# Performance work log

Measured on AMD Instinct MI355X. Metric: run time of the kernel, lower is better.

The kernel has to match this reference:

```python
import jax, jax.numpy as jnp
import numpy as np

N = 50000
E = 800000
IN_DIM, HID, OUT_DIM, HEADS = 256, 128, 64, 4


def _segment_sum(vals, ids, n):
    return jax.ops.segment_sum(vals, ids, num_segments=n)


def gcn_conv(x, src, dst, W, b, n):
    # PyG GCNConv: add self loops, symmetric normalization, aggregate at dst
    xw = x @ W  # [N, HID]
    loop = jnp.arange(n, dtype=src.dtype)
    srcA = jnp.concatenate([src, loop])
    dstA = jnp.concatenate([dst, loop])
    deg = _segment_sum(jnp.ones_like(srcA, dtype=xw.dtype), dstA, n)
    dinv = jnp.where(deg > 0, jax.lax.rsqrt(deg), 0.0)
    norm = dinv[srcA] * dinv[dstA]  # [E+N]
    msg = xw[srcA] * norm[:, None]  # [E+N, HID] -- dominant memory traffic
    return _segment_sum(msg, dstA, n) + b


def layer_norm(h, gamma, beta, eps=1e-5):
    mu = jnp.mean(h, axis=-1, keepdims=True)
    var = jnp.mean(jnp.square(h - mu), axis=-1, keepdims=True)
    return (h - mu) * jax.lax.rsqrt(var + eps) * gamma + beta


def gat_conv(x, src, dst, W, att_src, att_dst, b, n):
    # PyG GATConv (concat=True), self-loops added, eval mode (no dropout)
    xw = (x @ W).reshape(n, HEADS, HID)  # [N, H, C]
    a_s = jnp.sum(xw * att_src, axis=-1)  # [N, H]
    a_d = jnp.sum(xw * att_dst, axis=-1)  # [N, H]
    loop = jnp.arange(n, dtype=src.dtype)
    srcA = jnp.concatenate([src, loop])
    dstA = jnp.concatenate([dst, loop])
    e = jax.nn.leaky_relu(a_s[srcA] + a_d[dstA], 0.2)  # [E+N, H]
    m = jax.ops.segment_max(e, dstA, num_segments=n)  # [N, H]
    ex = jnp.exp(e - m[dstA])
    denom = _segment_sum(ex, dstA, n)  # [N, H] (>=1 entry per node via self loop)
    alpha = ex / denom[dstA]  # [E+N, H]
    msg = xw[srcA] * alpha[:, :, None]  # [E+N, H, C]
    out = _segment_sum(msg, dstA, n)  # [N, H, C]
    return out.reshape(n, HEADS * HID) + b


def setup_inputs() -> dict:
    key = jax.random.key(0)
    ks = jax.random.split(key, 16)
    x = jax.random.normal(ks[0], (N, IN_DIM), dtype=jnp.float32)
    edge_index = jax.random.randint(ks[1], (2, E), 0, N, dtype=jnp.int64)
    s = lambda k, shape, fan: jax.random.normal(k, shape, jnp.float32) / np.sqrt(fan)
    return {
        "x": x,
        "edge_index": edge_index,
        "Win": s(ks[2], (IN_DIM, HID), IN_DIM),
        "bin_": jnp.zeros((HID,), jnp.float32),
        "Wg1": s(ks[3], (HID, HID), HID),
        "bg1": jnp.zeros((HID,), jnp.float32),
        "g1_gamma": jnp.ones((HID,), jnp.float32),
        "g1_beta": jnp.zeros((HID,), jnp.float32),
        "Wg2": s(ks[4], (HID, HID), HID),
        "bg2": jnp.zeros((HID,), jnp.float32),
        "g2_gamma": jnp.ones((HID,), jnp.float32),
        "g2_beta": jnp.zeros((HID,), jnp.float32),
        "Wgat": s(ks[5], (HID, HEADS * HID), HID),
        "att_src": s(ks[6], (HEADS, HID), HID),
        "att_dst": s(ks[7], (HEADS, HID), HID),
        "bgat": jnp.zeros((HEADS * HID,), jnp.float32),
        "Watt_out": s(ks[8], (HEADS * HID, HID), HEADS * HID),
        "batt_out": jnp.zeros((HID,), jnp.float32),
        "Wout": s(ks[9], (HID, OUT_DIM), HID),
        "bout": jnp.zeros((OUT_DIM,), jnp.float32),
    }


def reference(x, edge_index, Win, bin_, Wg1, bg1, g1_gamma, g1_beta,
              Wg2, bg2, g2_gamma, g2_beta, Wgat, att_src, att_dst, bgat,
              Watt_out, batt_out, Wout, bout):
    src, dst = edge_index[0], edge_index[1]
    n = x.shape[0]
    # input projection (dropout = identity in eval)
    h0 = jax.nn.relu(x @ Win + bin_)
    # NOTE: original zip truncates -> only 2 of the 3 GCN layers execute.
    # layer 0 (i==0: no residual)
    h = gcn_conv(h0, src, dst, Wg1, bg1, n)
    h = jax.nn.relu(layer_norm(h, g1_gamma, g1_beta))
    x1 = h
    # layer 1 (i==1: residual)
    h = gcn_conv(x1, src, dst, Wg2, bg2, n)
    h = jax.nn.relu(layer_norm(h, g2_gamma, g2_beta))
    x2 = x1 + h
    # GAT attention block
    a = gat_conv(x2, src, dst, Wgat, att_src, att_dst, bgat, n)
    a = jax.nn.relu(a @ Watt_out + batt_out)
    # output projection
    return a @ Wout + bout
```

## Files before the change

kernel.cpp:

```cpp
#include <hip/hip_runtime.h>
#include <hip/hip_bf16.h>
#include <cstddef>
#include <cstdint>

#define TPB 256
#define HID 128
#define GATD 512
#define HEADS 4

typedef __attribute__((ext_vector_type(8))) short bf16x8;
typedef __attribute__((ext_vector_type(4))) float f32x4;

__device__ __forceinline__ float lrelu02(float x) { return x > 0.0f ? x : 0.2f * x; }

__device__ __forceinline__ unsigned short f2bf_rn(float f) {
  uint32_t u = __float_as_uint(f);
  u += 0x7fff + ((u >> 16) & 1);
  return (unsigned short)(u >> 16);
}
__device__ __forceinline__ float bf2f(unsigned short h) {
  return __uint_as_float(((uint32_t)h) << 16);
}
__device__ __forceinline__ float bflo(uint32_t u) { return __uint_as_float(u << 16); }
__device__ __forceinline__ float bfhi(uint32_t u) { return __uint_as_float(u & 0xffff0000u); }

__global__ void k_zero(int* __restrict__ p, int n) {
  int i = blockIdx.x * blockDim.x + threadIdx.x;
  if (i < n) p[i] = 0;
}

__global__ void k_hist(const int* __restrict__ dst, int* __restrict__ cnt, int E) {
  int i = blockIdx.x * blockDim.x + threadIdx.x;
  if (i < E) atomicAdd(&cnt[dst[i]], 1);
}

__global__ __launch_bounds__(256) void k_scan_blk(const int* __restrict__ cnt,
                                                  int* __restrict__ rowp,
                                                  int* __restrict__ bsum,
                                                  float* __restrict__ dinv, int n) {
  __shared__ int wsum[4];
  const int tid = threadIdx.x, lane = tid & 63, wid = tid >> 6;
  const int base = blockIdx.x * 1024 + tid * 4;
  int v[4];
#pragma unroll
  for (int q = 0; q < 4; ++q) {
    int idx = base + q;
    v[q] = (idx < n) ? cnt[idx] : 0;
    if (idx < n) dinv[idx] = rsqrtf((float)(v[q] + 1));
  }
  int s = v[0] + v[1] + v[2] + v[3];
  int sc = s;
#pragma unroll
  for (int off = 1; off < 64; off <<= 1) {
    int t = __shfl_up(sc, off);
    if (lane >= off) sc += t;
  }
  if (lane == 63) wsum[wid] = sc;
  __syncthreads();
  int woff = 0;
#pragma unroll
  for (int w = 0; w < 4; ++w)
    if (w < wid) woff += wsum[w];
  int run = woff + sc - s;
#pragma unroll
  for (int q = 0; q < 4; ++q) {
    int idx = base + q;
    if (idx < n) rowp[idx] = run;
    run += v[q];
  }
  if (tid == 255) bsum[blockIdx.x] = woff + sc;
}

__global__ __launch_bounds__(256) void k_scan_top(int* __restrict__ bsum, int nb) {
  __shared__ int sm[256];
  const int tid = threadIdx.x;
  int v = (tid < nb) ? bsum[tid] : 0;
  sm[tid] = v;
  __syncthreads();
  for (int off = 1; off < 256; off <<= 1) {
    int t = (tid >= off) ? sm[tid - off] : 0;
    __syncthreads();
    sm[tid] += t;
    __syncthreads();
  }
  int incl = sm[tid];
  if (tid < nb) bsum[tid] = incl - v;
  if (tid == nb - 1) bsum[nb] = incl;
}

__global__ void k_scan_add(int* __restrict__ rowp, const int* __restrict__ bsum,
                           int n, int nb) {
  int i = blockIdx.x * blockDim.x + threadIdx.x;
  if (i < n) rowp[i] += bsum[i >> 10];
  if (i == 0) rowp[n] = bsum[nb];
}

__global__ void k_fill(const int* __restrict__ src, const int* __restrict__ dst,
                       const int* __restrict__ rowp, int* __restrict__ cur,
                       int* __restrict__ colsrc, int E) {
  int i = blockIdx.x * blockDim.x + threadIdx.x;
  if (i < E) {
    int d = dst[i];
    int pos = rowp[d] + atomicAdd(&cur[d], 1);
    colsrc[pos] = src[i];
  }
}

__global__ void k_splitw_all(const float* __restrict__ Win, const float* __restrict__ Wg1,
                             const float* __restrict__ Wg2, const float* __restrict__ Wout,
                             unsigned short* __restrict__ WinTh, unsigned short* __restrict__ WinTl,
                             unsigned short* __restrict__ Wg1Th, unsigned short* __restrict__ Wg1Tl,
                             unsigned short* __restrict__ Wg2Th, unsigned short* __restrict__ Wg2Tl,
                             unsigned short* __restrict__ WoutTh, unsigned short* __restrict__ WoutTl) {
  int t = blockIdx.x * blockDim.x + threadIdx.x;
  const float* W;
  unsigned short *H, *L;
  int K, NC, r;
  if (t < 32768)      { W = Win;  H = WinTh;  L = WinTl;  K = 256; NC = 128; r = t; }
  else if (t < 49152) { W = Wg1;  H = Wg1Th;  L = Wg1Tl;  K = 128; NC = 128; r = t - 32768; }
  else if (t < 65536) { W = Wg2;  H = Wg2Th;  L = Wg2Tl;  K = 128; NC = 128; r = t - 49152; }
  else if (t < 73728) { W = Wout; H = WoutTh; L = WoutTl; K = 128; NC = 64;  r = t - 65536; }
  else return;
  int k = r / NC, n2 = r % NC;
  float v = W[r];
  unsigned short h = f2bf_rn(v);
  H[(size_t)n2 * K + k] = h;
  L[(size_t)n2 * K + k] = f2bf_rn(v - bf2f(h));
}

__global__ __launch_bounds__(256) void k_vprep(const float* __restrict__ Wgat,
                                               const float* __restrict__ Wao,
                                               unsigned short* __restrict__ VTh,
                                               unsigned short* __restrict__ VTl) {
  int t = blockIdx.x * blockDim.x + threadIdx.x;
  if (t >= 512 * 128) return;
  int j = t >> 7, k = t & 127;
  int c = j >> 2, h = j & 3;
  const float* wg = Wgat + (size_t)k * GATD + h * HID;
  const float* wa = Wao + (size_t)(h * HID) * HID + c;
  float s = 0.f;
#pragma unroll 4
  for (int d = 0; d < HID; ++d) s = fmaf(wg[d], wa[(size_t)d * HID], s);
  unsigned short hi = f2bf_rn(s);
  VTh[(size_t)j * HID + k] = hi;
  VTl[(size_t)j * HID + k] = f2bf_rn(s - bf2f(hi));
}

__global__ void k_cbias(const float* __restrict__ bgat, const float* __restrict__ Wao,
                        const float* __restrict__ bao, float* __restrict__ cb) {
  int c = threadIdx.x;
  if (c >= HID) return;
  float s = bao[c];
  for (int d = 0; d < GATD; ++d) s = fmaf(bgat[d], Wao[(size_t)d * HID + c], s);
  cb[c] = s;
}

template <int KTOT, int KC, int NCB, bool RELU, bool BIAS, int OUTM, int AMODE>
__global__ __launch_bounds__(256) void k_gemm5(
    const unsigned short* __restrict__ Ah, const unsigned short* __restrict__ Al,
    const unsigned short* __restrict__ BhT, const unsigned short* __restrict__ BlT,
    const float* __restrict__ bias, void* __restrict__ Cv, void* __restrict__ Cv2,
    int M, int NC) {
  constexpr int NSUB = KC / 32;
  constexpr int NCHUNK = KTOT / KC;
  constexpr int NCF = NCB / 16;
  constexpr int UNITS = NSUB * 2 * 4 * NCB;
  __shared__ alignas(16) unsigned short Bs[NSUB][2][4][NCB][8];
  const int tid = threadIdx.x, lane = tid & 63, wid = tid >> 6;
  const int m0 = blockIdx.x * 64;
  const int n0 = blockIdx.y * NCB;
  const int fr = lane & 15, g = lane >> 4;
  const int arow = m0 + wid * 16 + fr;
  const bool aok = arow < M;
  const size_t abase = (size_t)arow * KTOT;

  f32x4 acc[NCF];
#pragma unroll
  for (int cf = 0; cf < NCF; ++cf) acc[cf] = (f32x4){0.f, 0.f, 0.f, 0.f};

  for (int c = 0; c < NCHUNK; ++c) {
    const int c0 = c * KC;
    if (c > 0) __syncthreads();
#pragma unroll
    for (int it = 0; it < UNITS / 256; ++it) {
      const int u = tid + it * 256;
      const int n = u % NCB;
      int rest = u / NCB;
      const int kg = rest & 3;
      rest >>= 2;
      const int p = rest & 1;
      const int sub = rest >> 1;
      const unsigned short* sp =
          (p ? BlT : BhT) + (size_t)(n0 + n) * KTOT + c0 + sub * 32 + kg * 8;
      *(uint4*)&Bs[sub][p][kg][n][0] = *(const uint4*)sp;
    }
    __syncthreads();
#pragma unroll
    for (int sub = 0; sub < NSUB; ++sub) {
      const int kb = c0 + sub * 32 + g * 8;
      bf16x8 a_h = {}, a_l = {};
      if (aok) {
        if (AMODE == 0) {
          a_h = *(const bf16x8*)(Ah + abase + kb);
          a_l = *(const bf16x8*)(Al + abase + kb);
        } else {
          const float* Af = (const float*)Ah + abase + kb;
          float4 q0 = *(const float4*)Af;
          float4 q1 = *(const float4*)(Af + 4);
          float av[8] = {q0.x, q0.y, q0.z, q0.w, q1.x, q1.y, q1.z, q1.w};
          union { bf16x8 v; uint32_t u4[4]; } Hu, Lu;
#pragma unroll
          for (int q = 0; q < 4; ++q) {
            unsigned short h0 = f2bf_rn(av[2 * q]);
            unsigned short h1 = f2bf_rn(av[2 * q + 1]);
            unsigned short l0 = f2bf_rn(av[2 * q] - bf2f(h0));
            unsigned short l1 = f2bf_rn(av[2 * q + 1] - bf2f(h1));
            Hu.u4[q] = (uint32_t)h0 | ((uint32_t)h1 << 16);
            Lu.u4[q] = (uint32_t)l0 | ((uint32_t)l1 << 16);
          }
          a_h = Hu.v;
          a_l = Lu.v;
        }
      }
#pragma unroll
      for (int cf = 0; cf < NCF; ++cf) {
        bf16x8 b_h = *(const bf16x8*)&Bs[sub][0][g][cf * 16 + fr][0];
        bf16x8 b_l = *(const bf16x8*)&Bs[sub][1][g][cf * 16 + fr][0];
        acc[cf] = __builtin_amdgcn_mfma_f32_16x16x32_bf16(a_h, b_h, acc[cf], 0, 0, 0);
        acc[cf] = __builtin_amdgcn_mfma_f32_16x16x32_bf16(a_h, b_l, acc[cf], 0, 0, 0);
        acc[cf] = __builtin_amdgcn_mfma_f32_16x16x32_bf16(a_l, b_h, acc[cf], 0, 0, 0);
      }
    }
  }
#pragma unroll
  for (int cf = 0; cf < NCF; ++cf) {
    const int col = n0 + cf * 16 + fr;
    const float bv = BIAS ? bias[col] : 0.f;
#pragma unroll
    for (int r = 0; r < 4; ++r) {
      const int grow = m0 + wid * 16 + g * 4 + r;
      if (grow < M) {
        float v = acc[cf][r] + bv;
        if (RELU) v = fmaxf(v, 0.f);
        const size_t idx = (size_t)grow * NC + col;
        if (OUTM == 0) {
          ((float*)Cv)[idx] = v;
        } else if (OUTM == 1) {
          ((unsigned short*)Cv)[idx] = f2bf_rn(v);
        } else {
          unsigned short h = f2bf_rn(v);
          ((unsigned short*)Cv)[idx] = h;
          ((unsigned short*)Cv2)[idx] = f2bf_rn(v - bf2f(h));
        }
      }
    }
  }
}

template <bool L2>
__global__ __launch_bounds__(256) void k_gcn_agg(
    const unsigned short* __restrict__ xwb, const float* __restrict__ dinv,
    const int* __restrict__ rowp, const int* __restrict__ colsrc,
    const float* __restrict__ bias, const float* __restrict__ gamma,
    const float* __restrict__ beta,
    const unsigned short* __restrict__ resh, const unsigned short* __restrict__ resl,
    unsigned short* __restrict__ oh, unsigned short* __restrict__ ol,
    const float* __restrict__ waT, float* __restrict__ a_s, float* __restrict__ a_d,
    int n) {
  __shared__ float w[8][HID];
  if (L2) {
    for (int t = threadIdx.x; t < 8 * HID; t += 256) ((float*)w)[t] = waT[t];
    __syncthreads();
  }
  const int lane = threadIdx.x & 63;
  const int i = blockIdx.x * 4 + (threadIdx.x >> 6);
  if (i >= n) return;
  const float di = dinv[i];
  const int c = lane * 2;
  uint32_t v0 = *(const uint32_t*)(xwb + (size_t)i * HID + c);
  float a0 = bflo(v0) * di * di, a1 = bfhi(v0) * di * di;
  float b0 = 0.f, b1 = 0.f;
  const int e0 = rowp[i], e1 = rowp[i + 1];
  int j = e0;
  for (; j + 3 < e1; j += 4) {
    int s0 = colsrc[j], s1 = colsrc[j + 1], s2 = colsrc[j + 2], s3 = colsrc[j + 3];
    float w0 = dinv[s0] * di, w1 = dinv[s1] * di, w2 = dinv[s2] * di, w3 = dinv[s3] * di;
    uint32_t u0 = *(const uint32_t*)(xwb + (size_t)s0 * HID + c);
    uint32_t u1 = *(const uint32_t*)(xwb + (size_t)s1 * HID + c);
    uint32_t u2 = *(const uint32_t*)(xwb + (size_t)s2 * HID + c);
    uint32_t u3 = *(const uint32_t*)(xwb + (size_t)s3 * HID + c);
    a0 = fmaf(bflo(u0), w0, a0); a1 = fmaf(bfhi(u0), w0, a1);
    b0 = fmaf(bflo(u1), w1, b0); b1 = fmaf(bfhi(u1), w1, b1);
    a0 = fmaf(bflo(u2), w2, a0); a1 = fmaf(bfhi(u2), w2, a1);
    b0 = fmaf(bflo(u3), w3, b0); b1 = fmaf(bfhi(u3), w3, b1);
  }
  for (; j < e1; ++j) {
    int s0 = colsrc[j];
    float w0 = dinv[s0] * di;
    uint32_t u0 = *(const uint32_t*)(xwb + (size_t)s0 * HID + c);
    a0 = fmaf(bflo(u0), w0, a0);
    a1 = fmaf(bfhi(u0), w0, a1);
  }
  a0 += b0;
  a1 += b1;
  a0 += bias[c];
  a1 += bias[c + 1];
  float s1 = a0 + a1, s2 = a0 * a0 + a1 * a1;
#pragma unroll
  for (int m = 32; m >= 1; m >>= 1) {
    s1 += __shfl_xor(s1, m);
    s2 += __shfl_xor(s2, m);
  }
  float mu = s1 * (1.0f / HID);
  float var = s2 * (1.0f / HID) - mu * mu;
  float rstd = rsqrtf(var + 1e-5f);
  float y0 = fmaxf((a0 - mu) * rstd * gamma[c] + beta[c], 0.0f);
  float y1 = fmaxf((a1 - mu) * rstd * gamma[c + 1] + beta[c + 1], 0.0f);
  if (L2) {
    uint32_t rh = *(const uint32_t*)(resh + (size_t)i * HID + c);
    uint32_t rl = *(const uint32_t*)(resl + (size_t)i * HID + c);
    y0 += bflo(rh) + bflo(rl);
    y1 += bfhi(rh) + bfhi(rl);
  }
  unsigned short ph0 = f2bf_rn(y0), ph1 = f2bf_rn(y1);
  uint32_t hw = (uint32_t)ph0 | ((uint32_t)ph1 << 16);
  uint32_t lw = (uint32_t)f2bf_rn(y0 - bf2f(ph0)) |
                ((uint32_t)f2bf_rn(y1 - bf2f(ph1)) << 16);
  *(uint32_t*)(oh + (size_t)i * HID + c) = hw;
  *(uint32_t*)(ol + (size_t)i * HID + c) = lw;
  if (L2) {
    float p[8];
#pragma unroll
    for (int h = 0; h < 8; ++h) p[h] = y0 * w[h][c] + y1 * w[h][c + 1];
#pragma unroll
    for (int m = 32; m >= 1; m >>= 1) {
#pragma unroll
      for (int h = 0; h < 8; ++h) p[h] += __shfl_xor(p[h], m);
    }
    if (lane == 0) {
      a_s[i * 4 + 0] = p[0]; a_s[i * 4 + 1] = p[1];
      a_s[i * 4 + 2] = p[2]; a_s[i * 4 + 3] = p[3];
      a_d[i * 4 + 0] = p[4]; a_d[i * 4 + 1] = p[5];
      a_d[i * 4 + 2] = p[6]; a_d[i * 4 + 3] = p[7];
    }
  }
}

__global__ __launch_bounds__(256) void k_wprep(const float* __restrict__ Wgat,
                                               const float* __restrict__ att_src,
                                               const float* __restrict__ att_dst,
                                               float* __restrict__ waT) {
  int t = blockIdx.x * blockDim.x + threadIdx.x;
  if (t >= 1024) return;
  int p = t >> 7, k = t & 127;
  int h = p & 3;
  const float* av = (p < 4 ? att_src : att_dst) + h * HID;
  const float* wrow = Wgat + (size_t)k * GATD + h * HID;
  float s = 0.f;
#pragma unroll 4
  for (int c = 0; c < HID; ++c) s = fmaf(wrow[c], av[c], s);
  waT[t] = s;
}

__global__ __launch_bounds__(256) void k_gat_agg2(const unsigned short* __restrict__ zb,
                                                  const float* __restrict__ a_s,
                                                  const float* __restrict__ a_d,
                                                  const int* __restrict__ rowp,
                                                  const int* __restrict__ colsrc,
                                                  const float* __restrict__ cb,
                                                  unsigned short* __restrict__ atth,
                                                  unsigned short* __restrict__ attl,
                                                  int n) {
  __shared__ float4 albuf[4][64];
  __shared__ int sbuf[4][64];
  const int lane = threadIdx.x & 63;
  const int wid = threadIdx.x >> 6;
  const int i = blockIdx.x * 4 + wid;
  if (i >= n) return;
  const float4 adv = *(const float4*)(a_d + i * 4);
  const float4 asv = *(const float4*)(a_s + i * 4);
  float es0 = lrelu02(asv.x + adv.x);
  float es1 = lrelu02(asv.y + adv.y);
  float es2 = lrelu02(asv.z + adv.z);
  float es3 = lrelu02(asv.w + adv.w);
  const int e0 = rowp[i], e1 = rowp[i + 1];
  float m0 = es0, m1 = es1, m2 = es2, m3 = es3;
  for (int j = e0 + lane; j < e1; j += 64) {
    int s = colsrc[j];
    const float4 av = *(const float4*)(a_s + s * 4);
    m0 = fmaxf(m0, lrelu02(av.x + adv.x));
    m1 = fmaxf(m1, lrelu02(av.y + adv.y));
    m2 = fmaxf(m2, lrelu02(av.z + adv.z));
    m3 = fmaxf(m3, lrelu02(av.w + adv.w));
  }
#pragma unroll
  for (int m = 32; m >= 1; m >>= 1) {
    m0 = fmaxf(m0, __shfl_xor(m0, m));
    m1 = fmaxf(m1, __shfl_xor(m1, m));
    m2 = fmaxf(m2, __shfl_xor(m2, m));
    m3 = fmaxf(m3, __shfl_xor(m3, m));
  }
  float d0 = 0.f, d1 = 0.f, d2 = 0.f, d3 = 0.f;
  for (int j = e0 + lane; j < e1; j += 64) {
    int s = colsrc[j];
    const float4 av = *(const float4*)(a_s + s * 4);
    d0 += __expf(lrelu02(av.x + adv.x) - m0);
    d1 += __expf(lrelu02(av.y + adv.y) - m1);
    d2 += __expf(lrelu02(av.z + adv.z) - m2);
    d3 += __expf(lrelu02(av.w + adv.w) - m3);
  }
#pragma unroll
  for (int m = 32; m >= 1; m >>= 1) {
    d0 += __shfl_xor(d0, m);
    d1 += __shfl_xor(d1, m);
    d2 += __shfl_xor(d2, m);
    d3 += __shfl_xor(d3, m);
  }
  d0 += __expf(es0 - m0);
  d1 += __expf(es1 - m1);
  d2 += __expf(es2 - m2);
  d3 += __expf(es3 - m3);
  const float inv0 = 1.0f / d0, inv1 = 1.0f / d1, inv2 = 1.0f / d2, inv3 = 1.0f / d3;
  const float4 asf = make_float4(__expf(es0 - m0) * inv0, __expf(es1 - m1) * inv1,
                                 __expf(es2 - m2) * inv2, __expf(es3 - m3) * inv3);
  const int col8 = lane * 8;
  uint4 u = *(const uint4*)(zb + (size_t)i * GATD + col8);
  float4 accC0 = make_float4(bflo(u.x) * asf.x, bfhi(u.x) * asf.y,
                             bflo(u.y) * asf.z, bfhi(u.y) * asf.w);
  float4 accC1 = make_float4(bflo(u.z) * asf.x, bfhi(u.z) * asf.y,
                             bflo(u.w) * asf.z, bfhi(u.w) * asf.w);
  for (int b = e0; b < e1; b += 64) {
    int j = b + lane;
    if (j < e1) {
      int s = colsrc[j];
      const float4 av = *(const float4*)(a_s + s * 4);
      albuf[wid][lane] = make_float4(__expf(lrelu02(av.x + adv.x) - m0) * inv0,
                                     __expf(lrelu02(av.y + adv.y) - m1) * inv1,
                                     __expf(lrelu02(av.z + adv.z) - m2) * inv2,
                                     __expf(lrelu02(av.w + adv.w) - m3) * inv3);
      sbuf[wid][lane] = s;
    }
    asm volatile("s_waitcnt lgkmcnt(0)" ::: "memory");
    const int cnt = min(64, e1 - b);
    for (int t = 0; t < cnt; ++t) {
      float4 a4 = albuf[wid][t];
      int s = sbuf[wid][t];
      uint4 w = *(const uint4*)(zb + (size_t)s * GATD + col8);
      accC0.x = fmaf(bflo(w.x), a4.x, accC0.x);
      accC0.y = fmaf(bfhi(w.x), a4.y, accC0.y);
      accC0.z = fmaf(bflo(w.y), a4.z, accC0.z);
      accC0.w = fmaf(bfhi(w.y), a4.w, accC0.w);
      accC1.x = fmaf(bflo(w.z), a4.x, accC1.x);
      accC1.y = fmaf(bfhi(w.z), a4.y, accC1.y);
      accC1.z = fmaf(bflo(w.w), a4.z, accC1.z);
      accC1.w = fmaf(bfhi(w.w), a4.w, accC1.w);
    }
  }
  const int c0 = lane * 2;
  float2 cbv = *(const float2*)(cb + c0);
  float o0 = fmaxf(accC0.x + accC0.y + accC0.z + accC0.w + cbv.x, 0.0f);
  float o1 = fmaxf(accC1.x + accC1.y + accC1.z + accC1.w + cbv.y, 0.0f);
  unsigned short ph0 = f2bf_rn(o0), ph1 = f2bf_rn(o1);
  uint32_t hw = (uint32_t)ph0 | ((uint32_t)ph1 << 16);
  uint32_t lw = (uint32_t)f2bf_rn(o0 - bf2f(ph0)) |
                ((uint32_t)f2bf_rn(o1 - bf2f(ph1)) << 16);
  *(uint32_t*)(atth + (size_t)i * HID + c0) = hw;
  *(uint32_t*)(attl + (size_t)i * HID + c0) = lw;
}

extern "C" void kernel_launch(void* const* d_in, const int* in_sizes, int n_in,
                              void* d_out, int out_size, void* d_ws, size_t ws_size,
                              hipStream_t stream) {
  const float* x = (const float*)d_in[0];
  const int* ei = (const int*)d_in[1];
  const float* Win = (const float*)d_in[2];
  const float* bin = (const float*)d_in[3];
  const float* Wg1 = (const float*)d_in[4];
  const float* bg1 = (const float*)d_in[5];
  const float* g1g = (const float*)d_in[6];
  const float* g1b = (const float*)d_in[7];
  const float* Wg2 = (const float*)d_in[8];
  const float* bg2 = (const float*)d_in[9];
  const float* g2g = (const float*)d_in[10];
  const float* g2b = (const float*)d_in[11];
  const float* Wgat = (const float*)d_in[12];
  const float* att_s = (const float*)d_in[13];
  const float* att_d = (const float*)d_in[14];
  const float* bgat = (const float*)d_in[15];
  const float* Wao = (const float*)d_in[16];
  const float* bao = (const float*)d_in[17];
  const float* Wout = (const float*)d_in[18];
  const float* bout = (const float*)d_in[19];

  const int N = in_sizes[0] / 256;
  const int E = in_sizes[1] / 2;
  const int* src = ei;
  const int* dst = ei + E;

  char* base = (char*)d_ws;
  size_t off = 0;
  unsigned short* h0h = (unsigned short*)(base + off); off += (size_t)N * HID * 2;
  unsigned short* h0l = (unsigned short*)(base + off); off += (size_t)N * HID * 2;
  unsigned short* x1h = (unsigned short*)(base + off); off += (size_t)N * HID * 2;
  unsigned short* x1l = (unsigned short*)(base + off); off += (size_t)N * HID * 2;
  unsigned short* xwb = (unsigned short*)(base + off); off += (size_t)N * HID * 2;
  unsigned short* x2h = (unsigned short*)(base + off); off += (size_t)N * HID * 2;
  unsigned short* x2l = (unsigned short*)(base + off); off += (size_t)N * HID * 2;
  unsigned short* atth = x2h;
  unsigned short* attl = x2l;
  unsigned short* zb = (unsigned short*)(base + off); off += (size_t)N * GATD * 2;
  float* dinv = (float*)(base + off);                 off += (size_t)N * 4;
  float* a_s = (float*)(base + off);                  off += (size_t)N * 16;
  float* a_d = (float*)(base + off);                  off += (size_t)N * 16;
  float* waT = (float*)(base + off);                  off += 4096;
  float* cb = (float*)(base + off);                   off += 512;
  unsigned short *WinTh, *WinTl, *Wg1Th, *Wg1Tl, *Wg2Th, *Wg2Tl, *WoutTh, *WoutTl;
  unsigned short *VTh, *VTl;
  WinTh = (unsigned short*)(base + off);  off += 256 * 128 * 2;
  WinTl = (unsigned short*)(base + off);  off += 256 * 128 * 2;
  Wg1Th = (unsigned short*)(base + off);  off += 128 * 128 * 2;
  Wg1Tl = (unsigned short*)(base + off);  off += 128 * 128 * 2;
  Wg2Th = (unsigned short*)(base + off);  off += 128 * 128 * 2;
  Wg2Tl = (unsigned short*)(base + off);  off += 128 * 128 * 2;
  VTh = (unsigned short*)(base + off);    off += 512 * 128 * 2;
  VTl = (unsigned short*)(base + off);    off += 512 * 128 * 2;
  WoutTh = (unsigned short*)(base + off); off += 128 * 64 * 2;
  WoutTl = (unsigned short*)(base + off); off += 128 * 64 * 2;
  int* rowp = (int*)(base + off);   off += (size_t)(N + 1) * 4;
  int* colsrc = (int*)(base + off); off += (size_t)E * 4;
  const int nb2 = (N + 1023) / 1024;
  int* bsum = (int*)(base + off);   off += (size_t)(nb2 + 2) * 4;
  int* cnt = (int*)zb;
  int* cur = cnt + N;

  const int eb = (E + TPB - 1) / TPB;
  const int zbk = (2 * N + TPB - 1) / TPB;
  const int ab = (N + 3) / 4;
  const int gm = (N + 63) / 64;

  k_zero<<<zbk, TPB, 0, stream>>>(cnt, 2 * N);
  k_hist<<<eb, TPB, 0, stream>>>(dst, cnt, E);
  k_scan_blk<<<nb2, 256, 0, stream>>>(cnt, rowp, bsum, dinv, N);
  k_scan_top<<<1, 256, 0, stream>>>(bsum, nb2);
  k_scan_add<<<(N + 255) / 256, 256, 0, stream>>>(rowp, bsum, N, nb2);
  k_fill<<<eb, TPB, 0, stream>>>(src, dst, rowp, cur, colsrc, E);
  k_wprep<<<4, 256, 0, stream>>>(Wgat, att_s, att_d, waT);
  k_vprep<<<256, 256, 0, stream>>>(Wgat, Wao, VTh, VTl);
  k_cbias<<<1, 128, 0, stream>>>(bgat, Wao, bao, cb);
  k_splitw_all<<<(73728 + 255) / 256, 256, 0, stream>>>(
      Win, Wg1, Wg2, Wout, WinTh, WinTl, Wg1Th, Wg1Tl, Wg2Th, Wg2Tl, WoutTh, WoutTl);

  k_gemm5<256, 64, 128, true, true, 2, 1><<<dim3(gm, 1), 256, 0, stream>>>(
      (const unsigned short*)x, nullptr, WinTh, WinTl, bin, h0h, h0l, N, 128);
  k_gemm5<128, 64, 128, false, false, 1, 0><<<dim3(gm, 1), 256, 0, stream>>>(
      h0h, h0l, Wg1Th, Wg1Tl, nullptr, xwb, nullptr, N, 128);
  k_gcn_agg<false><<<ab, 256, 0, stream>>>(xwb, dinv, rowp, colsrc, bg1, g1g, g1b,
                                           nullptr, nullptr, x1h, x1l,
                                           nullptr, nullptr, nullptr, N);
  k_gemm5<128, 64, 128, false, false, 1, 0><<<dim3(gm, 1), 256, 0, stream>>>(
      x1h, x1l, Wg2Th, Wg2Tl, nullptr, xwb, nullptr, N, 128);
  k_gcn_agg<true><<<ab, 256, 0, stream>>>(xwb, dinv, rowp, colsrc, bg2, g2g, g2b,
                                          x1h, x1l, x2h, x2l, waT, a_s, a_d, N);
  k_gemm5<128, 32, 256, false, false, 1, 0><<<dim3(gm, 2), 256, 0, stream>>>(
      x2h, x2l, VTh, VTl, nullptr, zb, nullptr, N, 512);
  k_gat_agg2<<<ab, 256, 0, stream>>>(zb, a_s, a_d, rowp, colsrc, cb, atth, attl, N);
  k_gemm5<128, 128, 64, false, true, 0, 0><<<dim3(gm, 1), 256, 0, stream>>>(
      atth, attl, WoutTh, WoutTl, bout, d_out, nullptr, N, 64);
}
```

Baseline: 495.8 us.

## Fuse output projection into GAT aggregation and merge weight-prep kernels

The final Wout projection moves into the GAT aggregation kernel. Each wave writes its 128-wide attention row to shared memory and computes 64 fp32 outputs directly, so the bf16 hi/lo intermediate and a separate GEMM launch go away. Three small prep kernels are merged into one launch that also transposes Wout to fp32. The GCN aggregation gather loop is widened from 4 to 8 edges in flight to raise memory-level parallelism. In exchange, the output projection now runs on scalar FMAs instead of MFMA and rereads WoutT from cache for every node.

```diff
diff --git a/kernel.cpp b/kernel.cpp
--- a/kernel.cpp
+++ b/kernel.cpp
@@ -107,19 +107,17 @@
 }
 
 __global__ void k_splitw_all(const float* __restrict__ Win, const float* __restrict__ Wg1,
-                             const float* __restrict__ Wg2, const float* __restrict__ Wout,
+                             const float* __restrict__ Wg2,
                              unsigned short* __restrict__ WinTh, unsigned short* __restrict__ WinTl,
                              unsigned short* __restrict__ Wg1Th, unsigned short* __restrict__ Wg1Tl,
-                             unsigned short* __restrict__ Wg2Th, unsigned short* __restrict__ Wg2Tl,
-                             unsigned short* __restrict__ WoutTh, unsigned short* __restrict__ WoutTl) {
+                             unsigned short* __restrict__ Wg2Th, unsigned short* __restrict__ Wg2Tl) {
   int t = blockIdx.x * blockDim.x + threadIdx.x;
   const float* W;
   unsigned short *H, *L;
   int K, NC, r;
-  if (t < 32768)      { W = Win;  H = WinTh;  L = WinTl;  K = 256; NC = 128; r = t; }
-  else if (t < 49152) { W = Wg1;  H = Wg1Th;  L = Wg1Tl;  K = 128; NC = 128; r = t - 32768; }
-  else if (t < 65536) { W = Wg2;  H = Wg2Th;  L = Wg2Tl;  K = 128; NC = 128; r = t - 49152; }
-  else if (t < 73728) { W = Wout; H = WoutTh; L = WoutTl; K = 128; NC = 64;  r = t - 65536; }
+  if (t < 32768)      { W = Win; H = WinTh; L = WinTl; K = 256; NC = 128; r = t; }
+  else if (t < 49152) { W = Wg1; H = Wg1Th; L = Wg1Tl; K = 128; NC = 128; r = t - 32768; }
+  else if (t < 65536) { W = Wg2; H = Wg2Th; L = Wg2Tl; K = 128; NC = 128; r = t - 49152; }
   else return;
   int k = r / NC, n2 = r % NC;
   float v = W[r];
@@ -128,31 +126,50 @@
   L[(size_t)n2 * K + k] = f2bf_rn(v - bf2f(h));
 }
 
-__global__ __launch_bounds__(256) void k_vprep(const float* __restrict__ Wgat,
-                                               const float* __restrict__ Wao,
-                                               unsigned short* __restrict__ VTh,
-                                               unsigned short* __restrict__ VTl) {
+__global__ __launch_bounds__(256) void k_prep(const float* __restrict__ Wgat,
+                                              const float* __restrict__ att_src,
+                                              const float* __restrict__ att_dst,
+                                              const float* __restrict__ Wao,
+                                              const float* __restrict__ bgat,
+                                              const float* __restrict__ bao,
+                                              const float* __restrict__ Wout,
+                                              float* __restrict__ waT,
+                                              unsigned short* __restrict__ VTh,
+                                              unsigned short* __restrict__ VTl,
+                                              float* __restrict__ cb,
+                                              float* __restrict__ WoutT) {
   int t = blockIdx.x * blockDim.x + threadIdx.x;
-  if (t >= 512 * 128) return;
-  int j = t >> 7, k = t & 127;
-  int c = j >> 2, h = j & 3;
-  const float* wg = Wgat + (size_t)k * GATD + h * HID;
-  const float* wa = Wao + (size_t)(h * HID) * HID + c;
-  float s = 0.f;
+  if (t < 1024) {
+    int p = t >> 7, k = t & 127;
+    int h = p & 3;
+    const float* av = (p < 4 ? att_src : att_dst) + h * HID;
+    const float* wrow = Wgat + (size_t)k * GATD + h * HID;
+    float s = 0.f;
 #pragma unroll 4
-  for (int d = 0; d < HID; ++d) s = fmaf(wg[d], wa[(size_t)d * HID], s);
-  unsigned short hi = f2bf_rn(s);
-  VTh[(size_t)j * HID + k] = hi;
-  VTl[(size_t)j * HID + k] = f2bf_rn(s - bf2f(hi));
-}
-
-__global__ void k_cbias(const float* __restrict__ bgat, const float* __restrict__ Wao,
-                        const float* __restrict__ bao, float* __restrict__ cb) {
-  int c = threadIdx.x;
-  if (c >= HID) return;
-  float s = bao[c];
-  for (int d = 0; d < GATD; ++d) s = fmaf(bgat[d], Wao[(size_t)d * HID + c], s);
-  cb[c] = s;
+    for (int c = 0; c < HID; ++c) s = fmaf(wrow[c], av[c], s);
+    waT[t] = s;
+  } else if (t < 1024 + 65536) {
+    int r = t - 1024;
+    int j = r >> 7, k = r & 127;
+    int c = j >> 2, h = j & 3;
+    const float* wg = Wgat + (size_t)k * GATD + h * HID;
+    const float* wa = Wao + (size_t)(h * HID) * HID + c;
+    float s = 0.f;
+#pragma unroll 4
+    for (int d = 0; d < HID; ++d) s = fmaf(wg[d], wa[(size_t)d * HID], s);
+    unsigned short hi = f2bf_rn(s);
+    VTh[(size_t)j * HID + k] = hi;
+    VTl[(size_t)j * HID + k] = f2bf_rn(s - bf2f(hi));
+  } else if (t < 1024 + 65536 + 128) {
+    int c = t - 1024 - 65536;
+    float s = bao[c];
+    for (int d = 0; d < GATD; ++d) s = fmaf(bgat[d], Wao[(size_t)d * HID + c], s);
+    cb[c] = s;
+  } else if (t < 1024 + 65536 + 128 + 8192) {
+    int r = t - 1024 - 65536 - 128;
+    int cp = r >> 7, c = r & 127;
+    WoutT[(size_t)cp * HID + c] = Wout[(size_t)c * 64 + cp];
+  }
 }
 
 template <int KTOT, int KC, int NCB, bool RELU, bool BIAS, int OUTM, int AMODE>
@@ -282,17 +299,26 @@
   float b0 = 0.f, b1 = 0.f;
   const int e0 = rowp[i], e1 = rowp[i + 1];
   int j = e0;
-  for (; j + 3 < e1; j += 4) {
-    int s0 = colsrc[j], s1 = colsrc[j + 1], s2 = colsrc[j + 2], s3 = colsrc[j + 3];
-    float w0 = dinv[s0] * di, w1 = dinv[s1] * di, w2 = dinv[s2] * di, w3 = dinv[s3] * di;
-    uint32_t u0 = *(const uint32_t*)(xwb + (size_t)s0 * HID + c);
-    uint32_t u1 = *(const uint32_t*)(xwb + (size_t)s1 * HID + c);
-    uint32_t u2 = *(const uint32_t*)(xwb + (size_t)s2 * HID + c);
-    uint32_t u3 = *(const uint32_t*)(xwb + (size_t)s3 * HID + c);
-    a0 = fmaf(bflo(u0), w0, a0); a1 = fmaf(bfhi(u0), w0, a1);
-    b0 = fmaf(bflo(u1), w1, b0); b1 = fmaf(bfhi(u1), w1, b1);
-    a0 = fmaf(bflo(u2), w2, a0); a1 = fmaf(bfhi(u2), w2, a1);
-    b0 = fmaf(bflo(u3), w3, b0); b1 = fmaf(bfhi(u3), w3, b1);
+  for (; j + 7 < e1; j += 8) {
+    int ss[8];
+    float ww[8];
+    uint32_t uu[8];
+#pragma unroll
+    for (int q = 0; q < 8; ++q) ss[q] = colsrc[j + q];
+#pragma unroll
+    for (int q = 0; q < 8; ++q) ww[q] = dinv[ss[q]] * di;
+#pragma unroll
+    for (int q = 0; q < 8; ++q) uu[q] = *(const uint32_t*)(xwb + (size_t)ss[q] * HID + c);
+#pragma unroll
+    for (int q = 0; q < 8; ++q) {
+      if (q & 1) {
+        b0 = fmaf(bflo(uu[q]), ww[q], b0);
+        b1 = fmaf(bfhi(uu[q]), ww[q], b1);
+      } else {
+        a0 = fmaf(bflo(uu[q]), ww[q], a0);
+        a1 = fmaf(bfhi(uu[q]), ww[q], a1);
+      }
+    }
   }
   for (; j < e1; ++j) {
     int s0 = colsrc[j];
@@ -346,33 +372,19 @@
   }
 }
 
-__global__ __launch_bounds__(256) void k_wprep(const float* __restrict__ Wgat,
-                                               const float* __restrict__ att_src,
-                                               const float* __restrict__ att_dst,
-                                               float* __restrict__ waT) {
-  int t = blockIdx.x * blockDim.x + threadIdx.x;
-  if (t >= 1024) return;
-  int p = t >> 7, k = t & 127;
-  int h = p & 3;
-  const float* av = (p < 4 ? att_src : att_dst) + h * HID;
-  const float* wrow = Wgat + (size_t)k * GATD + h * HID;
-  float s = 0.f;
-#pragma unroll 4
-  for (int c = 0; c < HID; ++c) s = fmaf(wrow[c], av[c], s);
-  waT[t] = s;
-}
-
-__global__ __launch_bounds__(256) void k_gat_agg2(const unsigned short* __restrict__ zb,
+__global__ __launch_bounds__(256) void k_gat_agg3(const unsigned short* __restrict__ zb,
                                                   const float* __restrict__ a_s,
                                                   const float* __restrict__ a_d,
                                                   const int* __restrict__ rowp,
                                                   const int* __restrict__ colsrc,
                                                   const float* __restrict__ cb,
-                                                  unsigned short* __restrict__ atth,
-                                                  unsigned short* __restrict__ attl,
+                                                  const float* __restrict__ WoutT,
+                                                  const float* __restrict__ bout,
+                                                  float* __restrict__ outp,
                                                   int n) {
   __shared__ float4 albuf[4][64];
   __shared__ int sbuf[4][64];
+  __shared__ float attbuf[4][HID];
   const int lane = threadIdx.x & 63;
   const int wid = threadIdx.x >> 6;
   const int i = blockIdx.x * 4 + wid;
@@ -460,12 +472,20 @@
   float2 cbv = *(const float2*)(cb + c0);
   float o0 = fmaxf(accC0.x + accC0.y + accC0.z + accC0.w + cbv.x, 0.0f);
   float o1 = fmaxf(accC1.x + accC1.y + accC1.z + accC1.w + cbv.y, 0.0f);
-  unsigned short ph0 = f2bf_rn(o0), ph1 = f2bf_rn(o1);
-  uint32_t hw = (uint32_t)ph0 | ((uint32_t)ph1 << 16);
-  uint32_t lw = (uint32_t)f2bf_rn(o0 - bf2f(ph0)) |
-                ((uint32_t)f2bf_rn(o1 - bf2f(ph1)) << 16);
-  *(uint32_t*)(atth + (size_t)i * HID + c0) = hw;
-  *(uint32_t*)(attl + (size_t)i * HID + c0) = lw;
+  attbuf[wid][c0] = o0;
+  attbuf[wid][c0 + 1] = o1;
+  asm volatile("s_waitcnt lgkmcnt(0)" ::: "memory");
+  float acc = bout[lane];
+  const float* wrow = WoutT + (size_t)lane * HID;
+#pragma unroll 8
+  for (int c = 0; c < HID; c += 4) {
+    float4 wv = *(const float4*)(wrow + c);
+    acc = fmaf(attbuf[wid][c], wv.x, acc);
+    acc = fmaf(attbuf[wid][c + 1], wv.y, acc);
+    acc = fmaf(attbuf[wid][c + 2], wv.z, acc);
+    acc = fmaf(attbuf[wid][c + 3], wv.w, acc);
+  }
+  outp[(size_t)i * 64 + lane] = acc;
 }
 
 extern "C" void kernel_launch(void* const* d_in, const int* in_sizes, int n_in,
@@ -506,26 +526,22 @@
   unsigned short* xwb = (unsigned short*)(base + off); off += (size_t)N * HID * 2;
   unsigned short* x2h = (unsigned short*)(base + off); off += (size_t)N * HID * 2;
   unsigned short* x2l = (unsigned short*)(base + off); off += (size_t)N * HID * 2;
-  unsigned short* atth = x2h;
-  unsigned short* attl = x2l;
   unsigned short* zb = (unsigned short*)(base + off); off += (size_t)N * GATD * 2;
   float* dinv = (float*)(base + off);                 off += (size_t)N * 4;
   float* a_s = (float*)(base + off);                  off += (size_t)N * 16;
   float* a_d = (float*)(base + off);                  off += (size_t)N * 16;
   float* waT = (float*)(base + off);                  off += 4096;
   float* cb = (float*)(base + off);                   off += 512;
-  unsigned short *WinTh, *WinTl, *Wg1Th, *Wg1Tl, *Wg2Th, *Wg2Tl, *WoutTh, *WoutTl;
-  unsigned short *VTh, *VTl;
-  WinTh = (unsigned short*)(base + off);  off += 256 * 128 * 2;
-  WinTl = (unsigned short*)(base + off);  off += 256 * 128 * 2;
-  Wg1Th = (unsigned short*)(base + off);  off += 128 * 128 * 2;
-  Wg1Tl = (unsigned short*)(base + off);  off += 128 * 128 * 2;
-  Wg2Th = (unsigned short*)(base + off);  off += 128 * 128 * 2;
-  Wg2Tl = (unsigned short*)(base + off);  off += 128 * 128 * 2;
-  VTh = (unsigned short*)(base + off);    off += 512 * 128 * 2;
-  VTl = (unsigned short*)(base + off);    off += 512 * 128 * 2;
-  WoutTh = (unsigned short*)(base + off); off += 128 * 64 * 2;
-  WoutTl = (unsigned short*)(base + off); off += 128 * 64 * 2;
+  float* WoutT = (float*)(base + off);                off += 64 * 128 * 4;
+  unsigned short *WinTh, *WinTl, *Wg1Th, *Wg1Tl, *Wg2Th, *Wg2Tl, *VTh, *VTl;
+  WinTh = (unsigned short*)(base + off); off += 256 * 128 * 2;
+  WinTl = (unsigned short*)(base + off); off += 256 * 128 * 2;
+  Wg1Th = (unsigned short*)(base + off); off += 128 * 128 * 2;
+  Wg1Tl = (unsigned short*)(base + off); off += 128 * 128 * 2;
+  Wg2Th = (unsigned short*)(base + off); off += 128 * 128 * 2;
+  Wg2Tl = (unsigned short*)(base + off); off += 128 * 128 * 2;
+  VTh = (unsigned short*)(base + off);   off += 512 * 128 * 2;
+  VTl = (unsigned short*)(base + off);   off += 512 * 128 * 2;
   int* rowp = (int*)(base + off);   off += (size_t)(N + 1) * 4;
   int* colsrc = (int*)(base + off); off += (size_t)E * 4;
   const int nb2 = (N + 1023) / 1024;
@@ -544,11 +560,10 @@
   k_scan_top<<<1, 256, 0, stream>>>(bsum, nb2);
   k_scan_add<<<(N + 255) / 256, 256, 0, stream>>>(rowp, bsum, N, nb2);
   k_fill<<<eb, TPB, 0, stream>>>(src, dst, rowp, cur, colsrc, E);
-  k_wprep<<<4, 256, 0, stream>>>(Wgat, att_s, att_d, waT);
-  k_vprep<<<256, 256, 0, stream>>>(Wgat, Wao, VTh, VTl);
-  k_cbias<<<1, 128, 0, stream>>>(bgat, Wao, bao, cb);
-  k_splitw_all<<<(73728 + 255) / 256, 256, 0, stream>>>(
-      Win, Wg1, Wg2, Wout, WinTh, WinTl, Wg1Th, Wg1Tl, Wg2Th, Wg2Tl, WoutTh, WoutTl);
+  k_prep<<<(1024 + 65536 + 128 + 8192 + 255) / 256, 256, 0, stream>>>(
+      Wgat, att_s, att_d, Wao, bgat, bao, Wout, waT, VTh, VTl, cb, WoutT);
+  k_splitw_all<<<(65536 + 255) / 256, 256, 0, stream>>>(
+      Win, Wg1, Wg2, WinTh, WinTl, Wg1Th, Wg1Tl, Wg2Th, Wg2Tl);
 
   k_gemm5<256, 64, 128, true, true, 2, 1><<<dim3(gm, 1), 256, 0, stream>>>(
       (const unsigned short*)x, nullptr, WinTh, WinTl, bin, h0h, h0l, N, 128);
@@ -563,7 +578,6 @@
                                           x1h, x1l, x2h, x2l, waT, a_s, a_d, N);
   k_gemm5<128, 32, 256, false, false, 1, 0><<<dim3(gm, 2), 256, 0, stream>>>(
       x2h, x2l, VTh, VTl, nullptr, zb, nullptr, N, 512);
-  k_gat_agg2<<<ab, 256, 0, stream>>>(zb, a_s, a_d, rowp, colsrc, cb, atth, attl, N);
-  k_gemm5<128, 128, 64, false, true, 0, 0><<<dim3(gm, 1), 256, 0, stream>>>(
-      atth, attl, WoutTh, WoutTl, bout, d_out, nullptr, N, 64);
-}
+  k_gat_agg3<<<ab, 256, 0, stream>>>(zb, a_s, a_d, rowp, colsrc, cb, WoutT, bout,
+                                     (float*)d_out, N);
+}
```

Result: slower. 571.1 us (+15.2%).
